# Performance work log

Hardware: AMD Instinct MI355X
Metric: run time of the kernel (lower is better)

## Reference

```python
import jax, jax.numpy as jnp
import numpy as np

N_NODES = 100000

def _sage_conv(x, src, dst, W_l, b_l, W_r):
    # PyG SAGEConv(aggr='mean'): out = lin_l(mean_{j in N(i)} x_j) + lin_r(x_i)
    agg = jax.ops.segment_sum(x[src], dst, num_segments=N_NODES)          # [N, F]
    cnt = jax.ops.segment_sum(jnp.ones_like(dst, dtype=x.dtype), dst,
                              num_segments=N_NODES)                        # [N]
    mean = agg / jnp.maximum(cnt, 1.0)[:, None]
    return mean @ W_l + b_l + x @ W_r

def setup_inputs() -> dict:
    key = jax.random.key(0)
    ks = jax.random.split(key, 10)
    F_in, H = 128, 16
    E, P = 1600000, 2000000
    x = jax.random.normal(ks[0], (N_NODES, F_in), dtype=jnp.float32)
    edge_index = jax.random.randint(ks[1], (2, E), 0, N_NODES, dtype=jnp.int64)
    decode_index = jax.random.randint(ks[2], (2, P), 0, N_NODES, dtype=jnp.int64)
    s1 = 1.0 / np.sqrt(F_in)
    s2 = 1.0 / np.sqrt(H)
    W1l = jax.random.uniform(ks[3], (F_in, H), jnp.float32, -s1, s1)
    b1 = jax.random.uniform(ks[4], (H,), jnp.float32, -s1, s1)
    W1r = jax.random.uniform(ks[5], (F_in, H), jnp.float32, -s1, s1)
    W2l = jax.random.uniform(ks[6], (H, H), jnp.float32, -s2, s2)
    b2 = jax.random.uniform(ks[7], (H,), jnp.float32, -s2, s2)
    W2r = jax.random.uniform(ks[8], (H, H), jnp.float32, -s2, s2)
    return {"x": x, "W1l": W1l, "b1": b1, "W1r": W1r,
            "W2l": W2l, "b2": b2, "W2r": W2r,
            "edge_index": edge_index, "decode_index": decode_index}

def reference(x, W1l, b1, W1r, W2l, b2, W2r, edge_index, decode_index):
    src, dst = edge_index[0], edge_index[1]
    h = _sage_conv(x, src, dst, W1l, b1, W1r)          # conv1
    h = jax.nn.relu(h)                                  # relu (dropout: eval -> identity)
    h = _sage_conv(h, src, dst, W2l, b2, W2r)           # conv2
    logits = jnp.sum(h[decode_index[0]] * h[decode_index[1]], axis=1)  # [P]
    return jax.nn.sigmoid(logits)
```

## Files before the change

kernel.cpp:

```cpp
#include <hip/hip_runtime.h>
#include <hip/hip_fp16.h>

#define N_NODES 100000
#define F_IN 128
#define H 16
#define NBIN 391
#define BINCAP 4608
#define ECHUNK 8192
#define QSCALE 4096.0f
#define QINV (1.0f / 4096.0f)

__device__ inline unsigned int packi16(float a, float b) {
  int ia = __float2int_rn(fminf(fmaxf(a * QSCALE, -32767.f), 32767.f));
  int ib = __float2int_rn(fminf(fmaxf(b * QSCALE, -32767.f), 32767.f));
  return (unsigned int)((ia & 0xffff) | (ib << 16));
}

__device__ inline unsigned long long pk64(unsigned int w) {
  return ((unsigned long long)((w >> 16) ^ 0x8000u) << 32)
       | (unsigned long long)((w & 0xffffu) ^ 0x8000u);
}

__global__ void __launch_bounds__(512) k_init(int* __restrict__ binCur) {
  int t = threadIdx.x;
  if (t < NBIN) binCur[t] = t * BINCAP;
}

__global__ void __launch_bounds__(512) k_front(
    const float* __restrict__ x, const float* __restrict__ W1l,
    const float* __restrict__ W1r, unsigned short* __restrict__ y1l,
    float* __restrict__ y1r,
    const int* __restrict__ src, const int* __restrict__ dst,
    int* __restrict__ binCur, int* __restrict__ recs, int E, int fillB) {
  __shared__ __align__(16) char smem[49152];
  int t = threadIdx.x;
  int b = blockIdx.x;
  if (b < fillB) {
    int* hist = (int*)smem;
    int* gbase = hist + 512;
    int* cnt2 = gbase + 512;
    hist[t] = 0;
    cnt2[t] = 0;
    __syncthreads();
    int base = b * ECHUNK;
    int rec[16], bin[16];
#pragma unroll
    for (int j = 0; j < 16; ++j) {
      int e = base + j * 512 + t;
      if (e < E) {
        int s = src[e];
        int d = dst[e];
        rec[j] = (s << 8) | (d & 255);
        bin[j] = d >> 8;
        atomicAdd(&hist[bin[j]], 1);
      } else {
        bin[j] = -1;
      }
    }
    __syncthreads();
    if (t < NBIN) {
      int c = hist[t];
      gbase[t] = (c > 0) ? atomicAdd(&binCur[t], c) : 0;
    }
    __syncthreads();
#pragma unroll
    for (int j = 0; j < 16; ++j) {
      if (bin[j] >= 0) {
        int loc = atomicAdd(&cnt2[bin[j]], 1);
        int slot = gbase[bin[j]] + loc;
        if (slot < (bin[j] + 1) * BINCAP)
          recs[slot] = rec[j];
      }
    }
  } else {
    int lb = b - fillB;
    int wid = __builtin_amdgcn_readfirstlane(t >> 6);
    int part = wid & 3;
    int g = wid >> 2;
    int ln = t & 63;
    int n = lb * 128 + g * 64 + ln;
    int nc = (n < N_NODES) ? n : (N_NODES - 1);
    float* red = (float*)smem + g * 6144;
    const float4* xr = (const float4*)(x + (size_t)nc * F_IN + part * (F_IN / 4));
    float4 xv[8];
#pragma unroll
    for (int j = 0; j < 8; ++j) xv[j] = xr[j];
    const float* Wl = W1l + part * (F_IN / 4) * H;
    const float* Wr = W1r + part * (F_IN / 4) * H;
    float al[H], ar[H];
#pragma unroll
    for (int c = 0; c < H; ++c) { al[c] = 0.f; ar[c] = 0.f; }
#pragma unroll
    for (int j = 0; j < 8; ++j) {
      float xs[4] = {xv[j].x, xv[j].y, xv[j].z, xv[j].w};
#pragma unroll
      for (int jj = 0; jj < 4; ++jj) {
        int k = j * 4 + jj;
#pragma unroll
        for (int c = 0; c < H; ++c) {
          al[c] = fmaf(xs[jj], Wl[k * H + c], al[c]);
          ar[c] = fmaf(xs[jj], Wr[k * H + c], ar[c]);
        }
      }
    }
    if (part != 0) {
      int base = (part - 1) * 2048;
#pragma unroll
      for (int c = 0; c < H; ++c) {
        red[base + c * 64 + ln] = al[c];
        red[base + (H + c) * 64 + ln] = ar[c];
      }
    }
    __syncthreads();
    if (part == 0 && n < N_NODES) {
#pragma unroll
      for (int c = 0; c < H; ++c) {
        al[c] = ((al[c] + red[c * 64 + ln]) + red[2048 + c * 64 + ln])
                + red[4096 + c * 64 + ln];
        ar[c] = ((ar[c] + red[(H + c) * 64 + ln]) + red[2048 + (H + c) * 64 + ln])
                + red[4096 + (H + c) * 64 + ln];
      }
      uint4 w0, w1;
      w0.x = packi16(al[0], al[1]);  w0.y = packi16(al[2], al[3]);
      w0.z = packi16(al[4], al[5]);  w0.w = packi16(al[6], al[7]);
      w1.x = packi16(al[8], al[9]);  w1.y = packi16(al[10], al[11]);
      w1.z = packi16(al[12], al[13]); w1.w = packi16(al[14], al[15]);
      uint4* ol = (uint4*)(y1l + (size_t)n * H);
      ol[0] = w0;
      ol[1] = w1;
      float4* orr = (float4*)(y1r + (size_t)n * H);
#pragma unroll
      for (int q = 0; q < 4; ++q)
        orr[q] = make_float4(ar[4 * q], ar[4 * q + 1], ar[4 * q + 2], ar[4 * q + 3]);
    }
  }
}

__global__ void __launch_bounds__(512) k_agg1(
    const int* __restrict__ recs, const int* __restrict__ binCur,
    const unsigned short* __restrict__ y1l, const float* __restrict__ y1r,
    const float* __restrict__ b1, const float* __restrict__ W2l,
    const float* __restrict__ W2r, unsigned short* __restrict__ z2l,
    float* __restrict__ z2r) {
  __shared__ unsigned long long acc[8][256];
  __shared__ int cnt[256];
  __shared__ float hf[16][256];
  __shared__ float w2l[256];
  __shared__ float w2r[256];
  int t = threadIdx.x;
  int b = blockIdx.x;
#pragma unroll
  for (int j = 0; j < 4; ++j) ((unsigned long long*)acc)[j * 512 + t] = 0ULL;
  if (t < 256) { cnt[t] = 0; w2l[t] = W2l[t]; }
  else         w2r[t - 256] = W2r[t - 256];
  __syncthreads();
  int rbase = b * BINCAP;
  int R = binCur[b] - rbase;
  if (R > BINCAP) R = BINCAP;
  int rr[9];
#pragma unroll
  for (int j = 0; j < 9; ++j) {
    int idx = j * 512 + t;
    rr[j] = (idx < R) ? recs[rbase + idx] : -1;
  }
  uint4 va[9], vb[9];
#pragma unroll
  for (int j = 0; j < 9; ++j) {
    int s = (rr[j] >= 0) ? (rr[j] >> 8) : 0;
    const uint4* yp = (const uint4*)(y1l + (size_t)s * H);
    va[j] = yp[0];
    vb[j] = yp[1];
  }
#pragma unroll
  for (int j = 0; j < 9; ++j) {
    if (rr[j] >= 0) {
      int nb = rr[j] & 255;
      uint4 v0 = va[j], v1 = vb[j];
      atomicAdd(&cnt[nb], 1);
      atomicAdd(&acc[0][nb], pk64(v0.x));
      atomicAdd(&acc[1][nb], pk64(v0.y));
      atomicAdd(&acc[2][nb], pk64(v0.z));
      atomicAdd(&acc[3][nb], pk64(v0.w));
      atomicAdd(&acc[4][nb], pk64(v1.x));
      atomicAdd(&acc[5][nb], pk64(v1.y));
      atomicAdd(&acc[6][nb], pk64(v1.z));
      atomicAdd(&acc[7][nb], pk64(v1.w));
    }
  }
  __syncthreads();
  int node = t >> 1;
  int half = t & 1;
  int coff = half * 8;
  int n = (b << 8) + node;
  if (n < N_NODES) {
    int dg = cnt[node];
    unsigned int bias = (unsigned int)dg << 15;
    float s = QINV / fmaxf((float)dg, 1.f);
    const float4* yrp = (const float4*)(y1r + (size_t)n * H + coff);
    float4 y0 = yrp[0], y1v = yrp[1];
    const float4* bp = (const float4*)(b1 + coff);
    float4 b0 = bp[0], b1v = bp[1];
    float yv[8] = {y0.x, y0.y, y0.z, y0.w, y1v.x, y1v.y, y1v.z, y1v.w};
    float bv[8] = {b0.x, b0.y, b0.z, b0.w, b1v.x, b1v.y, b1v.z, b1v.w};
    int ia[8];
#pragma unroll
    for (int p = 0; p < 4; ++p) {
      unsigned long long a = acc[half * 4 + p][node];
      ia[2 * p]     = (int)((unsigned int)a - bias);
      ia[2 * p + 1] = (int)((unsigned int)(a >> 32) - bias);
    }
#pragma unroll
    for (int c = 0; c < 8; ++c) {
      float h = fmaf((float)ia[c], s, bv[c] + yv[c]);
      hf[coff + c][node] = fmaxf(h, 0.f);
    }
  } else {
#pragma unroll
    for (int c = 0; c < 8; ++c) hf[coff + c][node] = 0.f;
  }
  __syncthreads();
  float zl[8], zr[8];
#pragma unroll
  for (int c = 0; c < 8; ++c) { zl[c] = 0.f; zr[c] = 0.f; }
#pragma unroll
  for (int k = 0; k < 16; ++k) {
    float hk = hf[k][node];
#pragma unroll
    for (int c = 0; c < 8; ++c) {
      zl[c] = fmaf(hk, w2l[k * 16 + coff + c], zl[c]);
      zr[c] = fmaf(hk, w2r[k * 16 + coff + c], zr[c]);
    }
  }
  if (n < N_NODES) {
    uint4 pk;
    pk.x = packi16(zl[0], zl[1]);
    pk.y = packi16(zl[2], zl[3]);
    pk.z = packi16(zl[4], zl[5]);
    pk.w = packi16(zl[6], zl[7]);
    *(uint4*)(z2l + (size_t)n * H + coff) = pk;
    float4* zp = (float4*)(z2r + (size_t)n * H + coff);
    zp[0] = make_float4(zr[0], zr[1], zr[2], zr[3]);
    zp[1] = make_float4(zr[4], zr[5], zr[6], zr[7]);
  }
}

__global__ void __launch_bounds__(512) k_agg2(
    const int* __restrict__ recs, const int* __restrict__ binCur,
    const unsigned short* __restrict__ z2l, const float* __restrict__ z2r,
    const float* __restrict__ b2, __half* __restrict__ h2) {
  __shared__ unsigned long long acc[8][256];
  __shared__ int cnt[256];
  int t = threadIdx.x;
  int b = blockIdx.x;
#pragma unroll
  for (int j = 0; j < 4; ++j) ((unsigned long long*)acc)[j * 512 + t] = 0ULL;
  if (t < 256) cnt[t] = 0;
  __syncthreads();
  int rbase = b * BINCAP;
  int R = binCur[b] - rbase;
  if (R > BINCAP) R = BINCAP;
  int rr[9];
#pragma unroll
  for (int j = 0; j < 9; ++j) {
    int idx = j * 512 + t;
    rr[j] = (idx < R) ? recs[rbase + idx] : -1;
  }
  uint4 va[9], vb[9];
#pragma unroll
  for (int j = 0; j < 9; ++j) {
    int s = (rr[j] >= 0) ? (rr[j] >> 8) : 0;
    const uint4* yp = (const uint4*)(z2l + (size_t)s * H);
    va[j] = yp[0];
    vb[j] = yp[1];
  }
#pragma unroll
  for (int j = 0; j < 9; ++j) {
    if (rr[j] >= 0) {
      int nb = rr[j] & 255;
      uint4 v0 = va[j], v1 = vb[j];
      atomicAdd(&cnt[nb], 1);
      atomicAdd(&acc[0][nb], pk64(v0.x));
      atomicAdd(&acc[1][nb], pk64(v0.y));
      atomicAdd(&acc[2][nb], pk64(v0.z));
      atomicAdd(&acc[3][nb], pk64(v0.w));
      atomicAdd(&acc[4][nb], pk64(v1.x));
      atomicAdd(&acc[5][nb], pk64(v1.y));
      atomicAdd(&acc[6][nb], pk64(v1.z));
      atomicAdd(&acc[7][nb], pk64(v1.w));
    }
  }
  __syncthreads();
  int node = t >> 1;
  int half = t & 1;
  int coff = half * 8;
  int n = (b << 8) + node;
  if (n < N_NODES) {
    int dg = cnt[node];
    unsigned int bias = (unsigned int)dg << 15;
    float s = QINV / fmaxf((float)dg, 1.f);
    const float4* zrp = (const float4*)(z2r + (size_t)n * H + coff);
    float4 z0 = zrp[0], z1 = zrp[1];
    const float4* bp = (const float4*)(b2 + coff);
    float4 b0 = bp[0], b1v = bp[1];
    float zv[8] = {z0.x, z0.y, z0.z, z0.w, z1.x, z1.y, z1.z, z1.w};
    float bv[8] = {b0.x, b0.y, b0.z, b0.w, b1v.x, b1v.y, b1v.z, b1v.w};
    int ia[8];
#pragma unroll
    for (int p = 0; p < 4; ++p) {
      unsigned long long a = acc[half * 4 + p][node];
      ia[2 * p]     = (int)((unsigned int)a - bias);
      ia[2 * p + 1] = (int)((unsigned int)(a >> 32) - bias);
    }
    float v[8];
#pragma unroll
    for (int c = 0; c < 8; ++c)
      v[c] = fmaf((float)ia[c], s, bv[c] + zv[c]);
    __half2 h0 = __floats2half2_rn(v[0], v[1]);
    __half2 h1 = __floats2half2_rn(v[2], v[3]);
    __half2 h2p = __floats2half2_rn(v[4], v[5]);
    __half2 h3 = __floats2half2_rn(v[6], v[7]);
    uint4 pk;
    pk.x = *(unsigned int*)&h0;
    pk.y = *(unsigned int*)&h1;
    pk.z = *(unsigned int*)&h2p;
    pk.w = *(unsigned int*)&h3;
    *(uint4*)(h2 + (size_t)n * H + coff) = pk;
  }
}

__device__ inline float dot8h(uint4 u, uint4 v) {
  float acc = 0.f;
  const unsigned int* uw = (const unsigned int*)&u;
  const unsigned int* vw = (const unsigned int*)&v;
#pragma unroll
  for (int j = 0; j < 4; ++j) {
    float2 a = __half22float2(*(const __half2*)&uw[j]);
    float2 b = __half22float2(*(const __half2*)&vw[j]);
    acc = fmaf(a.x, b.x, acc);
    acc = fmaf(a.y, b.y, acc);
  }
  return acc;
}

__global__ void __launch_bounds__(256) k_decode(
    const int* __restrict__ ps, const int* __restrict__ pd,
    const __half* __restrict__ h2, float* __restrict__ out, int P) {
  int t = blockIdx.x * 256 + threadIdx.x;
  int p = t * 2;
  if (p >= P) return;
  int2 av = *(const int2*)(ps + p);
  int2 bv = *(const int2*)(pd + p);
  const uint4* ha0 = (const uint4*)(h2 + (size_t)av.x * H);
  const uint4* hb0 = (const uint4*)(h2 + (size_t)bv.x * H);
  const uint4* ha1 = (const uint4*)(h2 + (size_t)av.y * H);
  const uint4* hb1 = (const uint4*)(h2 + (size_t)bv.y * H);
  uint4 u00 = ha0[0], u01 = ha0[1];
  uint4 v00 = hb0[0], v01 = hb0[1];
  uint4 u10 = ha1[0], u11 = ha1[1];
  uint4 v10 = hb1[0], v11 = hb1[1];
  float d0 = dot8h(u00, v00) + dot8h(u01, v01);
  float d1 = dot8h(u10, v10) + dot8h(u11, v11);
  float o0 = 1.f / (1.f + __expf(-d0));
  float o1 = 1.f / (1.f + __expf(-d1));
  if (p + 1 < P) {
    *(float2*)(out + p) = make_float2(o0, o1);
  } else {
    out[p] = o0;
  }
}

extern "C" void kernel_launch(void* const* d_in, const int* in_sizes, int n_in,
                              void* d_out, int out_size, void* d_ws, size_t ws_size,
                              hipStream_t stream) {
  const float* x   = (const float*)d_in[0];
  const float* W1l = (const float*)d_in[1];
  const float* b1  = (const float*)d_in[2];
  const float* W1r = (const float*)d_in[3];
  const float* W2l = (const float*)d_in[4];
  const float* b2  = (const float*)d_in[5];
  const float* W2r = (const float*)d_in[6];
  const int* ei = (const int*)d_in[7];
  const int* di = (const int*)d_in[8];
  const int E = in_sizes[7] / 2;
  const int P = in_sizes[8] / 2;

  const size_t NF = (size_t)N_NODES * H;
  unsigned short* y1l = (unsigned short*)d_ws;
  __half*         h2  = (__half*)y1l;
  unsigned short* z2l = y1l + NF;
  float*  y1r = (float*)(z2l + NF);
  float*  z2r = y1r;
  int* recs   = (int*)(y1r + NF);
  int* binCur = recs + (size_t)NBIN * BINCAP;

  const int fillB = (E + ECHUNK - 1) / ECHUNK;
  const int lin1B = (N_NODES + 127) / 128;
  const int decodeBlocks = ((P + 1) / 2 + 255) / 256;

  k_init<<<1, 512, 0, stream>>>(binCur);
  k_front<<<fillB + lin1B, 512, 0, stream>>>(x, W1l, W1r, y1l, y1r,
                                             ei, ei + E, binCur, recs, E, fillB);
  k_agg1<<<NBIN, 512, 0, stream>>>(recs, binCur, y1l, y1r, b1, W2l, W2r,
                                   z2l, z2r);
  k_agg2<<<NBIN, 512, 0, stream>>>(recs, binCur, z2l, z2r, b2, h2);
  k_decode<<<decodeBlocks, 256, 0, stream>>>(di, di + P, h2, (float*)d_out, P);
}
```

Baseline: 197.6 us.

## Shrink destination bins to 64 nodes and widen decode to four pairs per thread

```diff
diff --git a/kernel.cpp b/kernel.cpp
--- a/kernel.cpp
+++ b/kernel.cpp
@@ -4,8 +4,8 @@
 #define N_NODES 100000
 #define F_IN 128
 #define H 16
-#define NBIN 391
-#define BINCAP 4608
+#define NBIN 1563
+#define BINCAP 1280
 #define ECHUNK 8192
 #define QSCALE 4096.0f
 #define QINV (1.0f / 4096.0f)
@@ -22,8 +22,8 @@
 }
 
 __global__ void __launch_bounds__(512) k_init(int* __restrict__ binCur) {
-  int t = threadIdx.x;
-  if (t < NBIN) binCur[t] = t * BINCAP;
+  int i = blockIdx.x * 512 + threadIdx.x;
+  if (i < NBIN) binCur[i] = i * BINCAP;
 }
 
 __global__ void __launch_bounds__(512) k_front(
@@ -37,10 +37,9 @@
   int b = blockIdx.x;
   if (b < fillB) {
     int* hist = (int*)smem;
-    int* gbase = hist + 512;
-    int* cnt2 = gbase + 512;
-    hist[t] = 0;
-    cnt2[t] = 0;
+    int* gbase = hist + NBIN;
+    int* cnt2 = gbase + NBIN;
+    for (int bb = t; bb < NBIN; bb += 512) { hist[bb] = 0; cnt2[bb] = 0; }
     __syncthreads();
     int base = b * ECHUNK;
     int rec[16], bin[16];
@@ -50,17 +49,17 @@
       if (e < E) {
         int s = src[e];
         int d = dst[e];
-        rec[j] = (s << 8) | (d & 255);
-        bin[j] = d >> 8;
+        rec[j] = (s << 6) | (d & 63);
+        bin[j] = d >> 6;
         atomicAdd(&hist[bin[j]], 1);
       } else {
         bin[j] = -1;
       }
     }
     __syncthreads();
-    if (t < NBIN) {
-      int c = hist[t];
-      gbase[t] = (c > 0) ? atomicAdd(&binCur[t], c) : 0;
+    for (int bb = t; bb < NBIN; bb += 512) {
+      int c = hist[bb];
+      if (c > 0) gbase[bb] = atomicAdd(&binCur[bb], c);
     }
     __syncthreads();
 #pragma unroll
@@ -142,105 +141,82 @@
     const float* __restrict__ b1, const float* __restrict__ W2l,
     const float* __restrict__ W2r, unsigned short* __restrict__ z2l,
     float* __restrict__ z2r) {
-  __shared__ unsigned long long acc[8][256];
-  __shared__ int cnt[256];
-  __shared__ float hf[16][256];
+  __shared__ unsigned long long acc[8][64];
+  __shared__ int cnt[64];
+  __shared__ float hf[16][64];
   __shared__ float w2l[256];
   __shared__ float w2r[256];
   int t = threadIdx.x;
   int b = blockIdx.x;
-#pragma unroll
-  for (int j = 0; j < 4; ++j) ((unsigned long long*)acc)[j * 512 + t] = 0ULL;
-  if (t < 256) { cnt[t] = 0; w2l[t] = W2l[t]; }
+  ((unsigned long long*)acc)[t] = 0ULL;
+  if (t < 64) cnt[t] = 0;
+  if (t < 256) w2l[t] = W2l[t];
   else         w2r[t - 256] = W2r[t - 256];
   __syncthreads();
   int rbase = b * BINCAP;
   int R = binCur[b] - rbase;
   if (R > BINCAP) R = BINCAP;
-  int rr[9];
-#pragma unroll
-  for (int j = 0; j < 9; ++j) {
+  int rc[3];
+  uint4 va[3], vb[3];
+#pragma unroll
+  for (int j = 0; j < 3; ++j) {
     int idx = j * 512 + t;
-    rr[j] = (idx < R) ? recs[rbase + idx] : -1;
-  }
-  uint4 va[9], vb[9];
-#pragma unroll
-  for (int j = 0; j < 9; ++j) {
-    int s = (rr[j] >= 0) ? (rr[j] >> 8) : 0;
+    rc[j] = (idx < R) ? recs[rbase + idx] : -1;
+  }
+#pragma unroll
+  for (int j = 0; j < 3; ++j) {
+    int s = (rc[j] >= 0) ? (rc[j] >> 6) : 0;
     const uint4* yp = (const uint4*)(y1l + (size_t)s * H);
     va[j] = yp[0];
     vb[j] = yp[1];
   }
 #pragma unroll
-  for (int j = 0; j < 9; ++j) {
-    if (rr[j] >= 0) {
-      int nb = rr[j] & 255;
-      uint4 v0 = va[j], v1 = vb[j];
+  for (int j = 0; j < 3; ++j) {
+    if (rc[j] >= 0) {
+      int nb = rc[j] & 63;
       atomicAdd(&cnt[nb], 1);
-      atomicAdd(&acc[0][nb], pk64(v0.x));
-      atomicAdd(&acc[1][nb], pk64(v0.y));
-      atomicAdd(&acc[2][nb], pk64(v0.z));
-      atomicAdd(&acc[3][nb], pk64(v0.w));
-      atomicAdd(&acc[4][nb], pk64(v1.x));
-      atomicAdd(&acc[5][nb], pk64(v1.y));
-      atomicAdd(&acc[6][nb], pk64(v1.z));
-      atomicAdd(&acc[7][nb], pk64(v1.w));
-    }
-  }
-  __syncthreads();
-  int node = t >> 1;
-  int half = t & 1;
-  int coff = half * 8;
-  int n = (b << 8) + node;
+      atomicAdd(&acc[0][nb], pk64(va[j].x));
+      atomicAdd(&acc[1][nb], pk64(va[j].y));
+      atomicAdd(&acc[2][nb], pk64(va[j].z));
+      atomicAdd(&acc[3][nb], pk64(va[j].w));
+      atomicAdd(&acc[4][nb], pk64(vb[j].x));
+      atomicAdd(&acc[5][nb], pk64(vb[j].y));
+      atomicAdd(&acc[6][nb], pk64(vb[j].z));
+      atomicAdd(&acc[7][nb], pk64(vb[j].w));
+    }
+  }
+  __syncthreads();
+  int node = t >> 3;
+  int q = t & 7;
+  int n = b * 64 + node;
+  float h0 = 0.f, h1 = 0.f;
   if (n < N_NODES) {
     int dg = cnt[node];
     unsigned int bias = (unsigned int)dg << 15;
     float s = QINV / fmaxf((float)dg, 1.f);
-    const float4* yrp = (const float4*)(y1r + (size_t)n * H + coff);
-    float4 y0 = yrp[0], y1v = yrp[1];
-    const float4* bp = (const float4*)(b1 + coff);
-    float4 b0 = bp[0], b1v = bp[1];
-    float yv[8] = {y0.x, y0.y, y0.z, y0.w, y1v.x, y1v.y, y1v.z, y1v.w};
-    float bv[8] = {b0.x, b0.y, b0.z, b0.w, b1v.x, b1v.y, b1v.z, b1v.w};
-    int ia[8];
-#pragma unroll
-    for (int p = 0; p < 4; ++p) {
-      unsigned long long a = acc[half * 4 + p][node];
-      ia[2 * p]     = (int)((unsigned int)a - bias);
-      ia[2 * p + 1] = (int)((unsigned int)(a >> 32) - bias);
-    }
-#pragma unroll
-    for (int c = 0; c < 8; ++c) {
-      float h = fmaf((float)ia[c], s, bv[c] + yv[c]);
-      hf[coff + c][node] = fmaxf(h, 0.f);
-    }
-  } else {
-#pragma unroll
-    for (int c = 0; c < 8; ++c) hf[coff + c][node] = 0.f;
-  }
-  __syncthreads();
-  float zl[8], zr[8];
-#pragma unroll
-  for (int c = 0; c < 8; ++c) { zl[c] = 0.f; zr[c] = 0.f; }
+    float2 yr = *(const float2*)(y1r + (size_t)n * H + 2 * q);
+    float2 bb = *(const float2*)(b1 + 2 * q);
+    unsigned long long a = acc[q][node];
+    int i0 = (int)((unsigned int)a - bias);
+    int i1 = (int)((unsigned int)(a >> 32) - bias);
+    h0 = fmaxf(fmaf((float)i0, s, bb.x + yr.x), 0.f);
+    h1 = fmaxf(fmaf((float)i1, s, bb.y + yr.y), 0.f);
+  }
+  hf[2 * q][node] = h0;
+  hf[2 * q + 1][node] = h1;
+  __syncthreads();
+  float zl0 = 0.f, zl1 = 0.f, zr0 = 0.f, zr1 = 0.f;
 #pragma unroll
   for (int k = 0; k < 16; ++k) {
     float hk = hf[k][node];
-#pragma unroll
-    for (int c = 0; c < 8; ++c) {
-      zl[c] = fmaf(hk, w2l[k * 16 + coff + c], zl[c]);
-      zr[c] = fmaf(hk, w2r[k * 16 + coff + c], zr[c]);
-    }
+    zl0 = fmaf(hk, w2l[k * 16 + 2 * q], zl0);
+    zl1 = fmaf(hk, w2l[k * 16 + 2 * q + 1], zl1);
+    zr0 = fmaf(hk, w2r[k * 16 + 2 * q], zr0);
+    zr1 = fmaf(hk, w2r[k * 16 + 2 * q + 1], zr1);
   }
   if (n < N_NODES) {
-    uint4 pk;
-    pk.x = packi16(zl[0], zl[1]);
-    pk.y = packi16(zl[2], zl[3]);
-    pk.z = packi16(zl[4], zl[5]);
-    pk.w = packi16(zl[6], zl[7]);
-    *(uint4*)(z2l + (size_t)n * H + coff) = pk;
-    float4* zp = (float4*)(z2r + (size_t)n * H + coff);
-    zp[0] = make_float4(zr[0], zr[1], zr[2], zr[3]);
-    zp[1] = make_float4(zr[4], zr[5], zr[6], zr[7]);
+    *(unsigned int*)(z2l + (size_t)n * H + 2 * q) = packi16(zl0, zl1);
+    *(float2*)(z2r + (size_t)n * H + 2 * q) = make_float2(zr0, zr1);
   }
 }
 
@@ -248,83 +224,62 @@
     const int* __restrict__ recs, const int* __restrict__ binCur,
     const unsigned short* __restrict__ z2l, const float* __restrict__ z2r,
     const float* __restrict__ b2, __half* __restrict__ h2) {
-  __shared__ unsigned long long acc[8][256];
-  __shared__ int cnt[256];
+  __shared__ unsigned long long acc[8][64];
+  __shared__ int cnt[64];
   int t = threadIdx.x;
   int b = blockIdx.x;
-#pragma unroll
-  for (int j = 0; j < 4; ++j) ((unsigned long long*)acc)[j * 512 + t] = 0ULL;
-  if (t < 256) cnt[t] = 0;
+  ((unsigned long long*)acc)[t] = 0ULL;
+  if (t < 64) cnt[t] = 0;
   __syncthreads();
   int rbase = b * BINCAP;
   int R = binCur[b] - rbase;
   if (R > BINCAP) R = BINCAP;
-  int rr[9];
-#pragma unroll
-  for (int j = 0; j < 9; ++j) {
+  int rc[3];
+  uint4 va[3], vb[3];
+#pragma unroll
+  for (int j = 0; j < 3; ++j) {
     int idx = j * 512 + t;
-    rr[j] = (idx < R) ? recs[rbase + idx] : -1;
-  }
-  uint4 va[9], vb[9];
-#pragma unroll
-  for (int j = 0; j < 9; ++j) {
-    int s = (rr[j] >= 0) ? (rr[j] >> 8) : 0;
+    rc[j] = (idx < R) ? recs[rbase + idx] : -1;
+  }
+#pragma unroll
+  for (int j = 0; j < 3; ++j) {
+    int s = (rc[j] >= 0) ? (rc[j] >> 6) : 0;
     const uint4* yp = (const uint4*)(z2l + (size_t)s * H);
     va[j] = yp[0];
     vb[j] = yp[1];
   }
 #pragma unroll
-  for (int j = 0; j < 9; ++j) {
-    if (rr[j] >= 0) {
-      int nb = rr[j] & 255;
-      uint4 v0 = va[j], v1 = vb[j];
+  for (int j = 0; j < 3; ++j) {
+    if (rc[j] >= 0) {
+      int nb = rc[j] & 63;
       atomicAdd(&cnt[nb], 1);
-      atomicAdd(&acc[0][nb], pk64(v0.x));
-      atomicAdd(&acc[1][nb], pk64(v0.y));
-      atomicAdd(&acc[2][nb], pk64(v0.z));
-      atomicAdd(&acc[3][nb], pk64(v0.w));
-      atomicAdd(&acc[4][nb], pk64(v1.x));
-      atomicAdd(&acc[5][nb], pk64(v1.y));
-      atomicAdd(&acc[6][nb], pk64(v1.z));
-      atomicAdd(&acc[7][nb], pk64(v1.w));
-    }
-  }
-  __syncthreads();
-  int node = t >> 1;
-  int half = t & 1;
-  int coff = half * 8;
-  int n = (b << 8) + node;
+      atomicAdd(&acc[0][nb], pk64(va[j].x));
+      atomicAdd(&acc[1][nb], pk64(va[j].y));
+      atomicAdd(&acc[2][nb], pk64(va[j].z));
+      atomicAdd(&acc[3][nb], pk64(va[j].w));
+      atomicAdd(&acc[4][nb], pk64(vb[j].x));
+      atomicAdd(&acc[5][nb], pk64(vb[j].y));
+      atomicAdd(&acc[6][nb], pk64(vb[j].z));
+      atomicAdd(&acc[7][nb], pk64(vb[j].w));
+    }
+  }
+  __syncthreads();
+  int node = t >> 3;
+  int q = t & 7;
+  int n = b * 64 + node;
   if (n < N_NODES) {
     int dg = cnt[node];
     unsigned int bias = (unsigned int)dg << 15;
     float s = QINV / fmaxf((float)dg, 1.f);
-    const float4* zrp = (const float4*)(z2r + (size_t)n * H + coff);
-    float4 z0 = zrp[0], z1 = zrp[1];
-    const float4* bp = (const float4*)(b2 + coff);
-    float4 b0 = bp[0], b1v = bp[1];
-    float zv[8] = {z0.x, z0.y, z0.z, z0.w, z1.x, z1.y, z1.z, z1.w};
-    float bv[8] = {b0.x, b0.y, b0.z, b0.w, b1v.x, b1v.y, b1v.z, b1v.w};
-    int ia[8];
-#pragma unroll
-    for (int p = 0; p < 4; ++p) {
-      unsigned long long a = acc[half * 4 + p][node];
-      ia[2 * p]     = (int)((unsigned int)a - bias);
-      ia[2 * p + 1] = (int)((unsigned int)(a >> 32) - bias);
-    }
-    float v[8];
-#pragma unroll
-    for (int c = 0; c < 8; ++c)
-      v[c] = fmaf((float)ia[c], s, bv[c] + zv[c]);
-    __half2 h0 = __floats2half2_rn(v[0], v[1]);
-    __half2 h1 = __floats2half2_rn(v[2], v[3]);
-    __half2 h2p = __floats2half2_rn(v[4], v[5]);
-    __half2 h3 = __floats2half2_rn(v[6], v[7]);
-    uint4 pk;
-    pk.x = *(unsigned int*)&h0;
-    pk.y = *(unsigned int*)&h1;
-    pk.z = *(unsigned int*)&h2p;
-    pk.w = *(unsigned int*)&h3;
-    *(uint4*)(h2 + (size_t)n * H + coff) = pk;
+    float2 zr = *(const float2*)(z2r + (size_t)n * H + 2 * q);
+    float2 bb = *(const float2*)(b2 + 2 * q);
+    unsigned long long a = acc[q][node];
+    int i0 = (int)((unsigned int)a - bias);
+    int i1 = (int)((unsigned int)(a >> 32) - bias);
+    float v0 = fmaf((float)i0, s, bb.x + zr.x);
+    float v1 = fmaf((float)i1, s, bb.y + zr.y);
+    __half2 hh = __floats2half2_rn(v0, v1);
+    *(unsigned int*)(h2 + (size_t)n * H + 2 * q) = *(unsigned int*)&hh;
   }
 }
 
@@ -346,26 +301,41 @@
     const int* __restrict__ ps, const int* __restrict__ pd,
     const __half* __restrict__ h2, float* __restrict__ out, int P) {
   int t = blockIdx.x * 256 + threadIdx.x;
-  int p = t * 2;
+  int p = t * 4;
   if (p >= P) return;
-  int2 av = *(const int2*)(ps + p);
-  int2 bv = *(const int2*)(pd + p);
-  const uint4* ha0 = (const uint4*)(h2 + (size_t)av.x * H);
-  const uint4* hb0 = (const uint4*)(h2 + (size_t)bv.x * H);
-  const uint4* ha1 = (const uint4*)(h2 + (size_t)av.y * H);
-  const uint4* hb1 = (const uint4*)(h2 + (size_t)bv.y * H);
-  uint4 u00 = ha0[0], u01 = ha0[1];
-  uint4 v00 = hb0[0], v01 = hb0[1];
-  uint4 u10 = ha1[0], u11 = ha1[1];
-  uint4 v10 = hb1[0], v11 = hb1[1];
-  float d0 = dot8h(u00, v00) + dot8h(u01, v01);
-  float d1 = dot8h(u10, v10) + dot8h(u11, v11);
-  float o0 = 1.f / (1.f + __expf(-d0));
-  float o1 = 1.f / (1.f + __expf(-d1));
-  if (p + 1 < P) {
-    *(float2*)(out + p) = make_float2(o0, o1);
+  if (p + 3 < P) {
+    int4 av = *(const int4*)(ps + p);
+    int4 bv = *(const int4*)(pd + p);
+    const int an[4] = {av.x, av.y, av.z, av.w};
+    const int bn[4] = {bv.x, bv.y, bv.z, bv.w};
+    uint4 ua[4][2], ub[4][2];
+#pragma unroll
+    for (int j = 0; j < 4; ++j) {
+      const uint4* ha = (const uint4*)(h2 + (size_t)an[j] * H);
+      const uint4* hb = (const uint4*)(h2 + (size_t)bn[j] * H);
+      ua[j][0] = ha[0]; ua[j][1] = ha[1];
+      ub[j][0] = hb[0]; ub[j][1] = hb[1];
+    }
+    float4 o;
+    float d;
+    d = dot8h(ua[0][0], ub[0][0]) + dot8h(ua[0][1], ub[0][1]);
+    o.x = 1.f / (1.f + __expf(-d));
+    d = dot8h(ua[1][0], ub[1][0]) + dot8h(ua[1][1], ub[1][1]);
+    o.y = 1.f / (1.f + __expf(-d));
+    d = dot8h(ua[2][0], ub[2][0]) + dot8h(ua[2][1], ub[2][1]);
+    o.z = 1.f / (1.f + __expf(-d));
+    d = dot8h(ua[3][0], ub[3][0]) + dot8h(ua[3][1], ub[3][1]);
+    o.w = 1.f / (1.f + __expf(-d));
+    *(float4*)(out + p) = o;
   } else {
-    out[p] = o0;
+    for (int k = 0; k < 4 && p + k < P; ++k) {
+      int a = ps[p + k];
+      int b = pd[p + k];
+      const uint4* ha = (const uint4*)(h2 + (size_t)a * H);
+      const uint4* hb = (const uint4*)(h2 + (size_t)b * H);
+      float d = dot8h(ha[0], hb[0]) + dot8h(ha[1], hb[1]);
+      out[p + k] = 1.f / (1.f + __expf(-d));
+    }
   }
 }
 
@@ -395,9 +365,10 @@
 
   const int fillB = (E + ECHUNK - 1) / ECHUNK;
   const int lin1B = (N_NODES + 127) / 128;
-  const int decodeBlocks = ((P + 1) / 2 + 255) / 256;
-
-  k_init<<<1, 512, 0, stream>>>(binCur);
+  const int initB = (NBIN + 511) / 512;
+  const int decodeBlocks = ((P + 3) / 4 + 255) / 256;
+
+  k_init<<<initB, 512, 0, stream>>>(binCur);
   k_front<<<fillB + lin1B, 512, 0, stream>>>(x, W1l, W1r, y1l, y1r,
                                              ei, ei + E, binCur, recs, E, fillB);
   k_agg1<<<NBIN, 512, 0, stream>>>(recs, binCur, y1l, y1r, b1, W2l, W2r,
```

Result: no change. 197.2 us (-0.2%).
